# Kernel optimization log

Measured on AMD Instinct MI355X. Metric: run time of the kernel, lower is better.

Reference implementation:

```python
import jax, jax.numpy as jnp
import numpy as np

B, T, H, W = 32, 100, 16, 16
CIN, HID, COUT, K = 64, 128, 64, 5
EPS = 1e-3      # keras LayerNormalization default epsilon
ALPHA = 0.2     # LeakyReLU slope


def _conv_same(x, w):
    # x: [B,H,W,Cin], w: [kh,kw,Cin,Cout] -> [B,H,W,Cout], SAME padding, stride 1
    return jax.lax.conv_general_dilated(
        x, w, window_strides=(1, 1), padding='SAME',
        dimension_numbers=('NHWC', 'HWIO', 'NHWC'))


def setup_inputs() -> dict:
    key = jax.random.key(0)
    ks = jax.random.split(key, 8)
    s = 0.05
    return {
        'initial_input': jax.random.normal(ks[0], (B, 1, H, W, CIN), jnp.float32),
        'h0': jax.random.normal(ks[1], (B, H, W, HID), jnp.float32) * s,
        'c0': jax.random.normal(ks[2], (B, H, W, HID), jnp.float32) * s,
        'targets': jax.random.normal(ks[3], (B, T, H, W, CIN), jnp.float32),
        'autoreg_prob': jnp.float32(0.5),
        # ConvLSTM2D params (keras gate order: i, f, c, o stacked on last axis)
        'Wx': jax.random.normal(ks[4], (K, K, CIN, 4 * HID), jnp.float32) * s,
        'Wh': jax.random.normal(ks[5], (K, K, HID, 4 * HID), jnp.float32) * s,
        'b': jnp.zeros((4 * HID,), jnp.float32),
        # Conv2D(64, 3, same)
        'conv_w': jax.random.normal(ks[6], (3, 3, HID, COUT), jnp.float32) * s,
        'conv_b': jnp.zeros((COUT,), jnp.float32),
        # LayerNorm (axis=-1)
        'gamma': jnp.ones((COUT,), jnp.float32),
        'beta': jnp.zeros((COUT,), jnp.float32),
    }


def reference(initial_input, h0, c0, targets, autoreg_prob,
              Wx, Wh, b, conv_w, conv_b, gamma, beta):
    T_ = targets.shape[1]
    t_switch = jnp.float32(T_) * autoreg_prob
    x0 = initial_input[:, 0]                       # [B,H,W,CIN] (seq-len-1 ConvLSTM step)
    tgt_t = jnp.transpose(targets, (1, 0, 2, 3, 4))  # [T,B,H,W,CIN]
    ts = jnp.arange(T_)

    def step(carry, inp):
        x, h, c = carry
        t, tgt = inp
        # ConvLSTM2D cell (one timestep)
        g = _conv_same(x, Wx) + _conv_same(h, Wh) + b   # [B,H,W,4*HID]
        i_g, f_g, c_g, o_g = jnp.split(g, 4, axis=-1)
        c = jax.nn.sigmoid(f_g) * c + jax.nn.sigmoid(i_g) * jnp.tanh(c_g)
        h = jax.nn.sigmoid(o_g) * jnp.tanh(c)
        # Conv2D -> LayerNorm(axis=-1) -> LeakyReLU(0.2)
        y = _conv_same(h, conv_w) + conv_b              # [B,H,W,COUT]
        mu = jnp.mean(y, axis=-1, keepdims=True)
        var = jnp.var(y, axis=-1, keepdims=True)
        y = (y - mu) * jax.lax.rsqrt(var + EPS) * gamma + beta
        out = jnp.where(y >= 0, y, ALPHA * y)
        # autoreg phase feeds output back; teacher phase feeds targets[:, t]
        next_x = jnp.where(t.astype(jnp.float32) < t_switch, out, tgt)
        return (next_x, h, c), out

    _, outs = jax.lax.scan(step, (x0, h0, c0), (ts, tgt_t))
    return jnp.transpose(outs, (1, 0, 2, 3, 4))        # [B,T,H,W,COUT]
```

## Files before the change

kernel.cpp:

```cpp
#include <hip/hip_runtime.h>

#define TT   100
#define PADW 20
#define HID  128
#define CIN  64
#define COUT 64
#define ALPHA 0.2f
#define LNEPS 1e-3f

typedef _Float16 f16;
typedef __attribute__((ext_vector_type(8))) _Float16 f16x8;
typedef __attribute__((ext_vector_type(4))) float f32x4;

__device__ __forceinline__ float fsig(float x) {
  return __builtin_amdgcn_rcpf(1.f + __builtin_amdgcn_exp2f(-1.44269504089f * x));
}
__device__ __forceinline__ float ftanh(float x) {
  return 1.f - 2.f * __builtin_amdgcn_rcpf(1.f + __builtin_amdgcn_exp2f(2.88539008178f * x));
}
__device__ __forceinline__ void gload16(const void* g, void* l) {
  __builtin_amdgcn_global_load_lds((const __attribute__((address_space(1))) void*)g,
                                   (__attribute__((address_space(3))) void*)l,
                                   16, 0, 0);
}

__global__ __launch_bounds__(512, 2) void kA(
    const f16* __restrict__ Xh, const f16* __restrict__ Xl,
    const f16* __restrict__ Hch, const f16* __restrict__ Hcl,
    f16* __restrict__ Hnh, f16* __restrict__ Hnl,
    const f16* __restrict__ Wch, const f16* __restrict__ Wcl,
    const float* __restrict__ bp, float* __restrict__ cst) {
  __shared__ __align__(16) f16 sAh[128][64];
  __shared__ __align__(16) f16 sAl[128][64];
  __shared__ __align__(16) f16 sBh[128][64];
  __shared__ __align__(16) f16 sBl[128][64];
  const int tid = threadIdx.x;
  const int l = tid & 63, w = tid >> 6;
  const int wm = w >> 2, wn = w & 3;
  const int mi = blockIdx.x, ni = blockIdx.y;
  const int cof = ((l & 7) ^ (l >> 3)) * 8;

  int posA[2], wBo[2];
#pragma unroll
  for (int i = 0; i < 2; ++i) {
    const int r = w * 16 + i * 8 + (l >> 3);
    const int m = mi * 128 + r;
    const int b = m >> 8, y = (m >> 4) & 15, x = m & 15;
    posA[i] = (b * PADW + y + 2) * PADW + (x + 2);
    wBo[i] = (ni * 128 + r) * 192 + cof;
  }

  f32x4 acc[4][2] = {};

  for (int it = 0; it < 75; ++it) {
    const int tap = it / 3, sub = it - tap * 3;
    const int dy = tap / 5, dx = tap - dy * 5;
    const int dt = (dy - 2) * PADW + (dx - 2);
    if (sub == 0) {
#pragma unroll
      for (int i = 0; i < 2; ++i) {
        gload16(Xh + (posA[i] + dt) * CIN + cof, &sAh[w * 16 + i * 8][0]);
        gload16(Xl + (posA[i] + dt) * CIN + cof, &sAl[w * 16 + i * 8][0]);
      }
    } else {
      const int ho = (sub - 1) * 64 + cof;
#pragma unroll
      for (int i = 0; i < 2; ++i) {
        gload16(Hch + (posA[i] + dt) * HID + ho, &sAh[w * 16 + i * 8][0]);
        gload16(Hcl + (posA[i] + dt) * HID + ho, &sAl[w * 16 + i * 8][0]);
      }
    }
    const int wo = tap * (512 * 192) + sub * 64;
#pragma unroll
    for (int i = 0; i < 2; ++i) {
      gload16(Wch + wBo[i] + wo, &sBh[w * 16 + i * 8][0]);
      gload16(Wcl + wBo[i] + wo, &sBl[w * 16 + i * 8][0]);
    }
    __syncthreads();
#pragma unroll
    for (int kk = 0; kk < 2; ++kk) {
      const int co = ((kk * 4 + (l >> 4)) ^ (l & 7)) * 8;
      f16x8 avh[4], avl[4], bvh[2], bvl[2];
#pragma unroll
      for (int fm = 0; fm < 4; ++fm) {
        avh[fm] = *(const f16x8*)&sAh[wm * 64 + fm * 16 + (l & 15)][co];
        avl[fm] = *(const f16x8*)&sAl[wm * 64 + fm * 16 + (l & 15)][co];
      }
#pragma unroll
      for (int fn = 0; fn < 2; ++fn) {
        bvh[fn] = *(const f16x8*)&sBh[wn * 32 + fn * 16 + (l & 15)][co];
        bvl[fn] = *(const f16x8*)&sBl[wn * 32 + fn * 16 + (l & 15)][co];
      }
#pragma unroll
      for (int fm = 0; fm < 4; ++fm)
#pragma unroll
        for (int fn = 0; fn < 2; ++fn) {
          acc[fm][fn] =
              __builtin_amdgcn_mfma_f32_16x16x32_f16(avh[fm], bvh[fn], acc[fm][fn], 0, 0, 0);
          acc[fm][fn] =
              __builtin_amdgcn_mfma_f32_16x16x32_f16(avl[fm], bvh[fn], acc[fm][fn], 0, 0, 0);
          acc[fm][fn] =
              __builtin_amdgcn_mfma_f32_16x16x32_f16(avh[fm], bvl[fn], acc[fm][fn], 0, 0, 0);
        }
    }
    __syncthreads();
  }

#pragma unroll
  for (int fn = 0; fn < 2; ++fn) {
    const int col = ni * 128 + wn * 32 + fn * 16 + (l & 15);
    const float bias = bp[col];
    const int ch = col >> 2;
#pragma unroll
    for (int fm = 0; fm < 4; ++fm) {
#pragma unroll
      for (int j = 0; j < 4; ++j) {
        const float v = acc[fm][fn][j] + bias;
        const float t1 = __shfl_xor(v, 1);
        const float t2 = __shfl_xor(v, 2);
        const float t3 = __shfl_xor(t1, 2);
        if ((l & 3) == 0) {
          const int m = mi * 128 + wm * 64 + fm * 16 + ((l >> 4) << 2) + j;
          const int cidx = m * HID + ch;
          const float cold = cst[cidx];
          const float cn = fsig(t1) * cold + fsig(v) * ftanh(t2);
          cst[cidx] = cn;
          const float h = fsig(t3) * ftanh(cn);
          const int b = m >> 8, y = (m >> 4) & 15, x = m & 15;
          const int pidx = ((b * PADW + y + 2) * PADW + (x + 2)) * HID + ch;
          const f16 hh = (f16)h;
          Hnh[pidx] = hh;
          Hnl[pidx] = (f16)(h - (float)hh);
        }
      }
    }
  }
}

__global__ __launch_bounds__(256, 2) void kB(
    const f16* __restrict__ Hnh, const f16* __restrict__ Hnl,
    const f16* __restrict__ Cwh, const f16* __restrict__ Cwl,
    const float* __restrict__ cb, const float* __restrict__ gam,
    const float* __restrict__ bet, const float* __restrict__ tgt,
    const float* __restrict__ prob, float* __restrict__ outp,
    f16* __restrict__ Xph, f16* __restrict__ Xpl, int t) {
  __shared__ __align__(16) f16 sAh[32][64];
  __shared__ __align__(16) f16 sAl[32][64];
  __shared__ __align__(16) f16 sBh[64][64];
  __shared__ __align__(16) f16 sBl[64][64];
  __shared__ __align__(16) float yl[32][68];
  const int tid = threadIdx.x;
  const int l = tid & 63, w = tid >> 6;
  const int wm = w >> 1, wn = w & 1;
  const int mi = blockIdx.x;
  const int cof = ((l & 7) ^ (l >> 3)) * 8;

  const int rA = w * 8 + (l >> 3);
  const int mA = mi * 32 + rA;
  const int bA = mA >> 8, yA = (mA >> 4) & 15, xA = mA & 15;
  const int posA = (bA * PADW + yA + 2) * PADW + (xA + 2);
  int wBo[2];
#pragma unroll
  for (int i = 0; i < 2; ++i) wBo[i] = (w * 16 + i * 8 + (l >> 3)) * HID + cof;

  f32x4 acc[2] = {};

  for (int it = 0; it < 18; ++it) {
    const int tap = it >> 1, sub = it & 1;
    const int dy = tap / 3, dx = tap - dy * 3;
    const int dt = (dy - 1) * PADW + (dx - 1);
    gload16(Hnh + (posA + dt) * HID + sub * 64 + cof, &sAh[w * 8][0]);
    gload16(Hnl + (posA + dt) * HID + sub * 64 + cof, &sAl[w * 8][0]);
    const int wo = tap * (64 * HID) + sub * 64;
#pragma unroll
    for (int i = 0; i < 2; ++i) {
      gload16(Cwh + wBo[i] + wo, &sBh[w * 16 + i * 8][0]);
      gload16(Cwl + wBo[i] + wo, &sBl[w * 16 + i * 8][0]);
    }
    __syncthreads();
#pragma unroll
    for (int kk = 0; kk < 2; ++kk) {
      const int co = ((kk * 4 + (l >> 4)) ^ (l & 7)) * 8;
      const f16x8 ah = *(const f16x8*)&sAh[wm * 16 + (l & 15)][co];
      const f16x8 al = *(const f16x8*)&sAl[wm * 16 + (l & 15)][co];
#pragma unroll
      for (int fn = 0; fn < 2; ++fn) {
        const f16x8 bh = *(const f16x8*)&sBh[wn * 32 + fn * 16 + (l & 15)][co];
        const f16x8 bl = *(const f16x8*)&sBl[wn * 32 + fn * 16 + (l & 15)][co];
        acc[fn] = __builtin_amdgcn_mfma_f32_16x16x32_f16(ah, bh, acc[fn], 0, 0, 0);
        acc[fn] = __builtin_amdgcn_mfma_f32_16x16x32_f16(al, bh, acc[fn], 0, 0, 0);
        acc[fn] = __builtin_amdgcn_mfma_f32_16x16x32_f16(ah, bl, acc[fn], 0, 0, 0);
      }
    }
    __syncthreads();
  }

#pragma unroll
  for (int fn = 0; fn < 2; ++fn) {
    const int col = wn * 32 + fn * 16 + (l & 15);
    const float bias = cb[col];
#pragma unroll
    for (int j = 0; j < 4; ++j) yl[wm * 16 + (l >> 4) * 4 + j][col] = acc[fn][j] + bias;
  }
  __syncthreads();

  if (tid < 128) {
    const int row = tid >> 2, part = tid & 3;
    f32x4 vv[4];
    float s = 0.f, q = 0.f;
#pragma unroll
    for (int k2 = 0; k2 < 4; ++k2) {
      vv[k2] = *(const f32x4*)&yl[row][part * 16 + k2 * 4];
#pragma unroll
      for (int e = 0; e < 4; ++e) { const float f = vv[k2][e]; s += f; q += f * f; }
    }
    s += __shfl_xor(s, 1); q += __shfl_xor(q, 1);
    s += __shfl_xor(s, 2); q += __shfl_xor(q, 2);
    const float mean = s * 0.015625f;
    const float var = q * 0.015625f - mean * mean;
    const float rs = __builtin_amdgcn_rsqf(fmaxf(var, 0.f) + LNEPS);
    const int m = mi * 32 + row;
    const int b = m >> 8, pos = m & 255;
    const int py = pos >> 4, px = pos & 15;
    const long obase = (((long)b * TT + t) * 256 + pos) * COUT + part * 16;
    float* op = outp + obase;
    const float* tp = tgt + obase;
    const bool ar = (float)t < 100.f * prob[0];
    const int xoff = ((b * PADW + py + 2) * PADW + px + 2) * CIN + part * 16;
    f16x8 ph[2], pl[2];
#pragma unroll
    for (int k2 = 0; k2 < 4; ++k2) {
      f32x4 o4;
#pragma unroll
      for (int e = 0; e < 4; ++e) {
        const int c = part * 16 + k2 * 4 + e;
        float val = (vv[k2][e] - mean) * rs * gam[c] + bet[c];
        val = val >= 0.f ? val : ALPHA * val;
        o4[e] = val;
        const float nxt = ar ? val : tp[k2 * 4 + e];
        const f16 nh = (f16)nxt;
        const int i16 = k2 * 4 + e;
        ph[i16 >> 3][i16 & 7] = nh;
        pl[i16 >> 3][i16 & 7] = (f16)(nxt - (float)nh);
      }
      *(f32x4*)(op + k2 * 4) = o4;
    }
    *(f16x8*)(Xph + xoff) = ph[0];
    *(f16x8*)(Xph + xoff + 8) = ph[1];
    *(f16x8*)(Xpl + xoff) = pl[0];
    *(f16x8*)(Xpl + xoff + 8) = pl[1];
  }
}

__global__ void k_wcomb(const float* __restrict__ Wx, const float* __restrict__ Wh,
                        f16* __restrict__ Wch, f16* __restrict__ Wcl) {
  const int idx = blockIdx.x * 256 + threadIdx.x;
  if (idx >= 25 * 512 * 192) return;
  const int c = idx % 192, r = idx / 192;
  const int n = r % 512, tap = r / 512;
  const int ch = n >> 2, g = n & 3, no = g * 128 + ch;
  const float v = (c < 64) ? Wx[(tap * 64 + c) * 512 + no]
                           : Wh[(tap * 128 + (c - 64)) * 512 + no];
  const f16 vh = (f16)v;
  Wch[idx] = vh;
  Wcl[idx] = (f16)(v - (float)vh);
}
__global__ void k_wconv(const float* __restrict__ cw, f16* __restrict__ Cwh,
                        f16* __restrict__ Cwl) {
  const int idx = blockIdx.x * 256 + threadIdx.x;
  if (idx >= 9 * 64 * 128) return;
  const int c = idx % 128, r = idx / 128;
  const int n = r % 64, tap = r / 64;
  const float v = cw[(tap * 128 + c) * 64 + n];
  const f16 vh = (f16)v;
  Cwh[idx] = vh;
  Cwl[idx] = (f16)(v - (float)vh);
}
__global__ void k_bperm(const float* __restrict__ b, float* __restrict__ bp) {
  const int n = blockIdx.x * 256 + threadIdx.x;
  if (n < 512) bp[n] = b[(n & 3) * 128 + (n >> 2)];
}
__global__ void k_init(const float* __restrict__ x0, const float* __restrict__ h0,
                       const float* __restrict__ c0, f16* __restrict__ Xph,
                       f16* __restrict__ Xpl, f16* __restrict__ Hh, f16* __restrict__ Hl,
                       float* __restrict__ cst) {
  const int idx = blockIdx.x * 256 + threadIdx.x;
  if (idx < 32 * 256 * 64) {
    const int ch = idx & 63, m = idx >> 6;
    const int b = m >> 8, y = (m >> 4) & 15, x = m & 15;
    const int p = ((b * PADW + y + 2) * PADW + x + 2) * CIN + ch;
    const float v = x0[idx];
    const f16 vh = (f16)v;
    Xph[p] = vh;
    Xpl[p] = (f16)(v - (float)vh);
  } else if (idx < 32 * 256 * 64 + 32 * 256 * 128) {
    const int j = idx - 32 * 256 * 64;
    const int ch = j & 127, m = j >> 7;
    const int b = m >> 8, y = (m >> 4) & 15, x = m & 15;
    const int p = ((b * PADW + y + 2) * PADW + x + 2) * HID + ch;
    const float v = h0[j];
    const f16 vh = (f16)v;
    Hh[p] = vh;
    Hl[p] = (f16)(v - (float)vh);
  } else if (idx < 32 * 256 * 64 + 2 * 32 * 256 * 128) {
    const int j = idx - 32 * 256 * 64 - 32 * 256 * 128;
    cst[j] = c0[j];
  }
}

extern "C" void kernel_launch(void* const* d_in, const int* in_sizes, int n_in,
                              void* d_out, int out_size, void* d_ws, size_t ws_size,
                              hipStream_t stream) {
  (void)in_sizes; (void)n_in; (void)out_size; (void)ws_size;
  const float* x0  = (const float*)d_in[0];
  const float* h0  = (const float*)d_in[1];
  const float* c0  = (const float*)d_in[2];
  const float* tgt = (const float*)d_in[3];
  const float* pr  = (const float*)d_in[4];
  const float* Wx  = (const float*)d_in[5];
  const float* Wh  = (const float*)d_in[6];
  const float* bb  = (const float*)d_in[7];
  const float* cw  = (const float*)d_in[8];
  const float* cbv = (const float*)d_in[9];
  const float* gam = (const float*)d_in[10];
  const float* bet = (const float*)d_in[11];
  float* outp = (float*)d_out;
  char* ws = (char*)d_ws;
  f16*   Xph = (f16*)(ws + 0);
  f16*   Xpl = (f16*)(ws + 1638400);
  f16*   Hh0 = (f16*)(ws + 3276800);
  f16*   Hl0 = (f16*)(ws + 6553600);
  f16*   Hh1 = (f16*)(ws + 9830400);
  f16*   Hl1 = (f16*)(ws + 13107200);
  float* cst = (float*)(ws + 16384000);
  f16*   Wch = (f16*)(ws + 20578304);
  f16*   Wcl = (f16*)(ws + 25493504);
  f16*   Cwh = (f16*)(ws + 30408704);
  f16*   Cwl = (f16*)(ws + 30556160);
  float* bp  = (float*)(ws + 30703616);

  hipMemsetAsync(Xph, 0, 1638400, stream);
  hipMemsetAsync(Xpl, 0, 1638400, stream);
  hipMemsetAsync(Hh0, 0, 3276800, stream);
  hipMemsetAsync(Hl0, 0, 3276800, stream);
  hipMemsetAsync(Hh1, 0, 3276800, stream);
  hipMemsetAsync(Hl1, 0, 3276800, stream);
  k_wcomb<<<9600, 256, 0, stream>>>(Wx, Wh, Wch, Wcl);
  k_wconv<<<288, 256, 0, stream>>>(cw, Cwh, Cwl);
  k_bperm<<<2, 256, 0, stream>>>(bb, bp);
  k_init<<<10240, 256, 0, stream>>>(x0, h0, c0, Xph, Xpl, Hh0, Hl0, cst);

  for (int t = 0; t < TT; ++t) {
    f16* hch = (t & 1) ? Hh1 : Hh0;
    f16* hcl = (t & 1) ? Hl1 : Hl0;
    f16* hnh = (t & 1) ? Hh0 : Hh1;
    f16* hnl = (t & 1) ? Hl0 : Hl1;
    kA<<<dim3(64, 4), 512, 0, stream>>>(Xph, Xpl, hch, hcl, hnh, hnl, Wch, Wcl, bp, cst);
    kB<<<256, 256, 0, stream>>>(hnh, hnl, Cwh, Cwl, cbv, gam, bet, tgt, pr, outp, Xph, Xpl, t);
  }
}
```

Measured before the change: 15.07 ms.

## Double-buffer LDS tiles in both GEMM kernels and remap kA blocks per XCD

Both the ConvLSTM gate kernel and the output-conv kernel now double-buffer their LDS tiles. The next K-slice is prefetched with async global-to-LDS loads while MFMAs run on the current slice, which removes one barrier per iteration. kA's 2D grid is flattened to 1D, and the block index is remapped so each XCD handles a single weight N-slice and contiguous M tiles, for better L2 reuse of weights. The doubled LDS (128KB in kA) forces launch_bounds down to one block per CU, which lowers occupancy.

```diff
diff --git a/kernel.cpp b/kernel.cpp
--- a/kernel.cpp
+++ b/kernel.cpp
@@ -24,20 +24,22 @@
                                    16, 0, 0);
 }
 
-__global__ __launch_bounds__(512, 2) void kA(
+__global__ __launch_bounds__(512, 1) void kA(
     const f16* __restrict__ Xh, const f16* __restrict__ Xl,
     const f16* __restrict__ Hch, const f16* __restrict__ Hcl,
     f16* __restrict__ Hnh, f16* __restrict__ Hnl,
     const f16* __restrict__ Wch, const f16* __restrict__ Wcl,
     const float* __restrict__ bp, float* __restrict__ cst) {
-  __shared__ __align__(16) f16 sAh[128][64];
-  __shared__ __align__(16) f16 sAl[128][64];
-  __shared__ __align__(16) f16 sBh[128][64];
-  __shared__ __align__(16) f16 sBl[128][64];
+  __shared__ __align__(16) f16 sAh[2][128][64];
+  __shared__ __align__(16) f16 sAl[2][128][64];
+  __shared__ __align__(16) f16 sBh[2][128][64];
+  __shared__ __align__(16) f16 sBl[2][128][64];
   const int tid = threadIdx.x;
   const int l = tid & 63, w = tid >> 6;
   const int wm = w >> 2, wn = w & 3;
-  const int mi = blockIdx.x, ni = blockIdx.y;
+  const int xcd = blockIdx.x & 7, slot = blockIdx.x >> 3;
+  const int ni = xcd >> 1;
+  const int mi = ((xcd & 1) << 5) + slot;
   const int cof = ((l & 7) ^ (l >> 3)) * 8;
 
   int posA[2], wBo[2];
@@ -50,46 +52,53 @@
     wBo[i] = (ni * 128 + r) * 192 + cof;
   }
 
-  f32x4 acc[4][2] = {};
-
-  for (int it = 0; it < 75; ++it) {
+  auto stage = [&](int bf, int it) {
     const int tap = it / 3, sub = it - tap * 3;
     const int dy = tap / 5, dx = tap - dy * 5;
     const int dt = (dy - 2) * PADW + (dx - 2);
     if (sub == 0) {
 #pragma unroll
       for (int i = 0; i < 2; ++i) {
-        gload16(Xh + (posA[i] + dt) * CIN + cof, &sAh[w * 16 + i * 8][0]);
-        gload16(Xl + (posA[i] + dt) * CIN + cof, &sAl[w * 16 + i * 8][0]);
+        gload16(Xh + (posA[i] + dt) * CIN + cof, &sAh[bf][w * 16 + i * 8][0]);
+        gload16(Xl + (posA[i] + dt) * CIN + cof, &sAl[bf][w * 16 + i * 8][0]);
       }
     } else {
       const int ho = (sub - 1) * 64 + cof;
 #pragma unroll
       for (int i = 0; i < 2; ++i) {
-        gload16(Hch + (posA[i] + dt) * HID + ho, &sAh[w * 16 + i * 8][0]);
-        gload16(Hcl + (posA[i] + dt) * HID + ho, &sAl[w * 16 + i * 8][0]);
+        gload16(Hch + (posA[i] + dt) * HID + ho, &sAh[bf][w * 16 + i * 8][0]);
+        gload16(Hcl + (posA[i] + dt) * HID + ho, &sAl[bf][w * 16 + i * 8][0]);
       }
     }
     const int wo = tap * (512 * 192) + sub * 64;
 #pragma unroll
     for (int i = 0; i < 2; ++i) {
-      gload16(Wch + wBo[i] + wo, &sBh[w * 16 + i * 8][0]);
-      gload16(Wcl + wBo[i] + wo, &sBl[w * 16 + i * 8][0]);
-    }
-    __syncthreads();
+      gload16(Wch + wBo[i] + wo, &sBh[bf][w * 16 + i * 8][0]);
+      gload16(Wcl + wBo[i] + wo, &sBl[bf][w * 16 + i * 8][0]);
+    }
+  };
+
+  f32x4 acc[4][2] = {};
+
+  stage(0, 0);
+  __syncthreads();
+
+  int buf = 0;
+  for (int it = 0; it < 75; ++it) {
+    if (it < 74) stage(buf ^ 1, it + 1);
 #pragma unroll
     for (int kk = 0; kk < 2; ++kk) {
       const int co = ((kk * 4 + (l >> 4)) ^ (l & 7)) * 8;
       f16x8 avh[4], avl[4], bvh[2], bvl[2];
 #pragma unroll
       for (int fm = 0; fm < 4; ++fm) {
-        avh[fm] = *(const f16x8*)&sAh[wm * 64 + fm * 16 + (l & 15)][co];
-        avl[fm] = *(const f16x8*)&sAl[wm * 64 + fm * 16 + (l & 15)][co];
+        avh[fm] = *(const f16x8*)&sAh[buf][wm * 64 + fm * 16 + (l & 15)][co];
+        avl[fm] = *(const f16x8*)&sAl[buf][wm * 64 + fm * 16 + (l & 15)][co];
       }
 #pragma unroll
       for (int fn = 0; fn < 2; ++fn) {
-        bvh[fn] = *(const f16x8*)&sBh[wn * 32 + fn * 16 + (l & 15)][co];
-        bvl[fn] = *(const f16x8*)&sBl[wn * 32 + fn * 16 + (l & 15)][co];
+        bvh[fn] = *(const f16x8*)&sBh[buf][wn * 32 + fn * 16 + (l & 15)][co];
+        bvl[fn] = *(const f16x8*)&sBl[buf][wn * 32 + fn * 16 + (l & 15)][co];
       }
 #pragma unroll
       for (int fm = 0; fm < 4; ++fm)
@@ -104,6 +113,7 @@
         }
     }
     __syncthreads();
+    buf ^= 1;
   }
 
 #pragma unroll
@@ -144,10 +154,10 @@
     const float* __restrict__ bet, const float* __restrict__ tgt,
     const float* __restrict__ prob, float* __restrict__ outp,
     f16* __restrict__ Xph, f16* __restrict__ Xpl, int t) {
-  __shared__ __align__(16) f16 sAh[32][64];
-  __shared__ __align__(16) f16 sAl[32][64];
-  __shared__ __align__(16) f16 sBh[64][64];
-  __shared__ __align__(16) f16 sBl[64][64];
+  __shared__ __align__(16) f16 sAh[2][32][64];
+  __shared__ __align__(16) f16 sAl[2][32][64];
+  __shared__ __align__(16) f16 sBh[2][64][64];
+  __shared__ __align__(16) f16 sBl[2][64][64];
   __shared__ __align__(16) float yl[32][68];
   const int tid = threadIdx.x;
   const int l = tid & 63, w = tid >> 6;
@@ -163,36 +173,44 @@
 #pragma unroll
   for (int i = 0; i < 2; ++i) wBo[i] = (w * 16 + i * 8 + (l >> 3)) * HID + cof;
 
-  f32x4 acc[2] = {};
-
-  for (int it = 0; it < 18; ++it) {
+  auto stage = [&](int bf, int it) {
     const int tap = it >> 1, sub = it & 1;
     const int dy = tap / 3, dx = tap - dy * 3;
     const int dt = (dy - 1) * PADW + (dx - 1);
-    gload16(Hnh + (posA + dt) * HID + sub * 64 + cof, &sAh[w * 8][0]);
-    gload16(Hnl + (posA + dt) * HID + sub * 64 + cof, &sAl[w * 8][0]);
+    gload16(Hnh + (posA + dt) * HID + sub * 64 + cof, &sAh[bf][w * 8][0]);
+    gload16(Hnl + (posA + dt) * HID + sub * 64 + cof, &sAl[bf][w * 8][0]);
     const int wo = tap * (64 * HID) + sub * 64;
 #pragma unroll
     for (int i = 0; i < 2; ++i) {
-      gload16(Cwh + wBo[i] + wo, &sBh[w * 16 + i * 8][0]);
-      gload16(Cwl + wBo[i] + wo, &sBl[w * 16 + i * 8][0]);
-    }
-    __syncthreads();
+      gload16(Cwh + wBo[i] + wo, &sBh[bf][w * 16 + i * 8][0]);
+      gload16(Cwl + wBo[i] + wo, &sBl[bf][w * 16 + i * 8][0]);
+    }
+  };
+
+  f32x4 acc[2] = {};
+
+  stage(0, 0);
+  __syncthreads();
+
+  int buf = 0;
+  for (int it = 0; it < 18; ++it) {
+    if (it < 17) stage(buf ^ 1, it + 1);
 #pragma unroll
     for (int kk = 0; kk < 2; ++kk) {
       const int co = ((kk * 4 + (l >> 4)) ^ (l & 7)) * 8;
-      const f16x8 ah = *(const f16x8*)&sAh[wm * 16 + (l & 15)][co];
-      const f16x8 al = *(const f16x8*)&sAl[wm * 16 + (l & 15)][co];
+      const f16x8 ah = *(const f16x8*)&sAh[buf][wm * 16 + (l & 15)][co];
+      const f16x8 al = *(const f16x8*)&sAl[buf][wm * 16 + (l & 15)][co];
 #pragma unroll
       for (int fn = 0; fn < 2; ++fn) {
-        const f16x8 bh = *(const f16x8*)&sBh[wn * 32 + fn * 16 + (l & 15)][co];
-        const f16x8 bl = *(const f16x8*)&sBl[wn * 32 + fn * 16 + (l & 15)][co];
+        const f16x8 bh = *(const f16x8*)&sBh[buf][wn * 32 + fn * 16 + (l & 15)][co];
+        const f16x8 bl = *(const f16x8*)&sBl[buf][wn * 32 + fn * 16 + (l & 15)][co];
         acc[fn] = __builtin_amdgcn_mfma_f32_16x16x32_f16(ah, bh, acc[fn], 0, 0, 0);
         acc[fn] = __builtin_amdgcn_mfma_f32_16x16x32_f16(al, bh, acc[fn], 0, 0, 0);
         acc[fn] = __builtin_amdgcn_mfma_f32_16x16x32_f16(ah, bl, acc[fn], 0, 0, 0);
       }
     }
     __syncthreads();
+    buf ^= 1;
   }
 
 #pragma unroll
@@ -355,7 +373,7 @@
     f16* hcl = (t & 1) ? Hl1 : Hl0;
     f16* hnh = (t & 1) ? Hh0 : Hh1;
     f16* hnl = (t & 1) ? Hl0 : Hl1;
-    kA<<<dim3(64, 4), 512, 0, stream>>>(Xph, Xpl, hch, hcl, hnh, hnl, Wch, Wcl, bp, cst);
+    kA<<<256, 512, 0, stream>>>(Xph, Xpl, hch, hcl, hnh, hnl, Wch, Wcl, bp, cst);
     kB<<<256, 256, 0, stream>>>(hnh, hnl, Cwh, Cwl, cbv, gam, bet, tgt, pr, outp, Xph, Xpl, t);
   }
 }
```

New measurement: 14.70 ms. 1.03x faster.
